# Optimization experiments

Hardware: AMD Instinct MI355X
Metric: run time of the kernel (lower is better)

The kernel has to match this reference:

```python
import jax, jax.numpy as jnp
import numpy as np

B, N, H, E_PER = 32, 128, 128, 4096  # graphs, nodes/graph, hidden_dim, pairs/graph


def setup_inputs() -> dict:
    key = jax.random.key(0)
    k1, k2, k3, k4, k5 = jax.random.split(key, 5)
    h_node = jax.random.normal(k1, (B, N, H), dtype=jnp.float32)
    h_edge = jax.random.normal(k2, (B, N, N, H), dtype=jnp.float32)
    # pairlist rows (b, i, j), grouped by batch index b as the torch loop assumes
    b = jnp.repeat(jnp.arange(B, dtype=jnp.int32), E_PER)
    i = jax.random.randint(k3, (B * E_PER,), 0, N, dtype=jnp.int32)
    j = jax.random.randint(k4, (B * E_PER,), 0, N, dtype=jnp.int32)
    pairlist = jnp.stack([b, i, j], axis=1)
    # foward_message_layer: Linear(3H, 6H); store weight transposed for x @ W
    W = jax.random.normal(k5, (3 * H, 6 * H), dtype=jnp.float32) / np.float32(np.sqrt(3 * H))
    bias = jnp.zeros((6 * H,), dtype=jnp.float32)
    return {"h_node": h_node, "h_edge": h_edge, "pairlist": pairlist, "W": W, "bias": bias}


def reference(h_node, h_edge, pairlist, W, bias):
    # Gather per-pair node/edge embeddings and concat: [E, 3H]
    bi, ii, jj = pairlist[:, 0], pairlist[:, 1], pairlist[:, 2]
    m = jnp.concatenate(
        [h_node[bi, ii], h_node[bi, jj], h_edge[bi, ii, jj]], axis=-1
    )
    # Shared linear message transform (Linear(3H, 6H)), then regroup per graph
    out = m @ W + bias  # [E, 6H]
    return out.reshape(B, E_PER, 6 * H)
```

## Files before the change

### kernel.cpp

```cpp
#include <hip/hip_runtime.h>


#define NNODE 128
#define HDIM  128
#define KDIM  384
#define NOUT  768
#define BM    128
#define BN    128
#define BK    64
#define NKITER 6

typedef __attribute__((ext_vector_type(4))) float f32x4;
typedef __attribute__((ext_vector_type(8))) short bf16x8;

static __device__ __forceinline__ short f2b(float f) {
    return __builtin_bit_cast(short, (__bf16)f);
}

static __device__ __forceinline__ void gload_lds16(const void* g, void* l) {
    __builtin_amdgcn_global_load_lds((const __attribute__((address_space(1))) void*)g,
                                     (__attribute__((address_space(3))) void*)l, 16, 0, 0);
}

__global__ void prep_kernel(const float* __restrict__ W, short* __restrict__ WtS) {
    int gid  = blockIdx.x * 256 + threadIdx.x;
    int tile = gid >> 10;
    int c    = gid & 1023;
    int nb   = tile / 6, kk = tile - nb * 6;
    int row  = c >> 3;
    int kb   = (c & 7) ^ (row & 7);
    int n    = nb * 128 + row;
    int k0   = kk * 64 + kb * 8;
    short v[8];
    #pragma unroll
    for (int e = 0; e < 8; ++e) v[e] = f2b(W[(k0 + e) * NOUT + n]);
    *(bf16x8*)(WtS + (size_t)gid * 8) = *(bf16x8*)v;
}

__global__ __launch_bounds__(256) void gemm_kernel(
    const float* __restrict__ h_node, const float* __restrict__ h_edge,
    const int* __restrict__ pl, const short* __restrict__ WtS,
    const float* __restrict__ bias, float* __restrict__ out) {

    __shared__ int rowOff[3][BM];
    __shared__ __align__(16) short Abuf[2][BM * BK];
    __shared__ __align__(16) short Bbuf[2][BN * BK];

    const int tid = threadIdx.x;
    const int bid = blockIdx.x;
    const int xcd = bid & 7;
    const int idx = bid >> 3;
    const int mBase = (xcd * 128 + idx / 6) * BM;
    const int nb    = idx % 6;
    const int nBase = nb * BN;
    const int nb6   = nb * 6;

    if (tid < BM) {
        int e  = pl ? mBase + tid : 0;
        int b  = pl[3 * (mBase + tid) + 0];
        int ii = pl[3 * (mBase + tid) + 1];
        int jj = pl[3 * (mBase + tid) + 2];
        (void)e;
        rowOff[0][tid] = (b * NNODE + ii) * HDIM;
        rowOff[1][tid] = (b * NNODE + jj) * HDIM;
        rowOff[2][tid] = ((b * NNODE + ii) * NNODE + jj) * HDIM;
    }
    __syncthreads();

    const int lane = tid & 63;
    const int wid  = tid >> 6;
    const int wm   = wid & 1;
    const int wn   = wid >> 1;
    const int r    = lane & 15;
    const int g    = lane >> 4;
    const int srow = tid >> 3;
    const int sc   = tid & 7;

    int ro[3][4];
    #pragma unroll
    for (int s = 0; s < 3; ++s)
        #pragma unroll
        for (int t = 0; t < 4; ++t)
            ro[s][t] = rowOff[s][srow + t * 32];

    f32x4 acc[4][4];
    #pragma unroll
    for (int a = 0; a < 4; ++a)
        #pragma unroll
        for (int b2 = 0; b2 < 4; ++b2)
            acc[a][b2] = (f32x4){0.f, 0.f, 0.f, 0.f};

    f32x4 a0[4], a1[4];

    auto issueA = [&](int kt) {
        const int seg  = kt >> 1;
        const float* gb = (seg < 2) ? h_node : h_edge;
        const int koff = (kt & 1) * BK;
        #pragma unroll
        for (int t = 0; t < 4; ++t) {
            const float* p = gb + ro[seg][t] + koff + sc * 8;
            a0[t] = *(const f32x4*)p;
            a1[t] = *(const f32x4*)(p + 4);
        }
    };
    auto issueB = [&](int kt, int buf) {
        const short* src = WtS + (size_t)((nb6 + kt) << 10) * 8;
        short* ldsb = &Bbuf[buf][0];
        #pragma unroll
        for (int i = 0; i < 4; ++i) {
            int cb0 = wid * 256 + i * 64;
            gload_lds16(src + (size_t)(cb0 + lane) * 8, ldsb + cb0 * 8);
        }
    };
    auto writeA = [&](int buf) {
        char* Ab = (char*)&Abuf[buf][0];
        #pragma unroll
        for (int t = 0; t < 4; ++t) {
            int row  = srow + t * 32;
            int byte = (row * 128 + sc * 16) ^ ((row & 7) << 4);
            bf16x8 v;
            v[0] = f2b(a0[t][0]); v[1] = f2b(a0[t][1]);
            v[2] = f2b(a0[t][2]); v[3] = f2b(a0[t][3]);
            v[4] = f2b(a1[t][0]); v[5] = f2b(a1[t][1]);
            v[6] = f2b(a1[t][2]); v[7] = f2b(a1[t][3]);
            *(bf16x8*)(Ab + byte) = v;
        }
    };
    auto compute = [&](int buf) {
        char* Ab = (char*)&Abuf[buf][0];
        char* Bb = (char*)&Bbuf[buf][0];
        #pragma unroll
        for (int ks = 0; ks < 2; ++ks) {
            const int cb = ks * 4 + g;
            bf16x8 ef[4], wf[4];
            #pragma unroll
            for (int mf = 0; mf < 4; ++mf) {
                int row  = wm * 64 + mf * 16 + r;
                int byte = (row * 128 + cb * 16) ^ ((row & 7) << 4);
                ef[mf] = *(const bf16x8*)(Ab + byte);
            }
            #pragma unroll
            for (int nf = 0; nf < 4; ++nf) {
                int row  = wn * 64 + nf * 16 + r;
                int byte = (row * 128 + cb * 16) ^ ((row & 7) << 4);
                wf[nf] = *(const bf16x8*)(Bb + byte);
            }
            #pragma unroll
            for (int nf = 0; nf < 4; ++nf)
                #pragma unroll
                for (int mf = 0; mf < 4; ++mf)
                    acc[nf][mf] = __builtin_amdgcn_mfma_f32_16x16x32_bf16(
                        wf[nf], ef[mf], acc[nf][mf], 0, 0, 0);
        }
    };

    issueA(0);
    issueB(0, 0);
    asm volatile("s_waitcnt vmcnt(0)" ::: "memory");
    writeA(0);
    __syncthreads();

    int cur = 0;
    #pragma unroll
    for (int t = 0; t < NKITER; ++t) {
        if (t + 1 < NKITER) {
            issueA(t + 1);
            issueB(t + 1, cur ^ 1);
        }
        compute(cur);
        if (t + 1 < NKITER) {
            asm volatile("s_waitcnt vmcnt(0)" ::: "memory");
            writeA(cur ^ 1);
            __syncthreads();
        }
        cur ^= 1;
    }

    #pragma unroll
    for (int nf = 0; nf < 4; ++nf) {
        int n = nBase + wn * 64 + nf * 16 + g * 4;
        f32x4 bb = *(const f32x4*)(bias + n);
        #pragma unroll
        for (int mf = 0; mf < 4; ++mf) {
            int m = mBase + wm * 64 + mf * 16 + r;
            f32x4 v = acc[nf][mf] + bb;
            *(f32x4*)(out + (size_t)m * NOUT + n) = v;
        }
    }
}

extern "C" void kernel_launch(void* const* d_in, const int* in_sizes, int n_in,
                              void* d_out, int out_size, void* d_ws, size_t ws_size,
                              hipStream_t stream) {
    const float* h_node = (const float*)d_in[0];
    const float* h_edge = (const float*)d_in[1];
    const int*   pl     = (const int*)d_in[2];
    const float* W      = (const float*)d_in[3];
    const float* bias   = (const float*)d_in[4];
    float* out = (float*)d_out;
    short* WtS = (short*)d_ws;

    prep_kernel<<<144, 256, 0, stream>>>(W, WtS);
    gemm_kernel<<<1024 * 6, 256, 0, stream>>>(h_node, h_edge, pl, WtS, bias, out);
}
```

Measured before the change: 636.1 us.

## Split gather into separate bf16 pre-pass and stage A via direct LDS loads

Result: slower. 662.4 us (+4.1%).

```diff
diff --git a/kernel.cpp b/kernel.cpp
--- a/kernel.cpp
+++ b/kernel.cpp
@@ -9,6 +9,7 @@
 #define BN    128
 #define BK    64
 #define NKITER 6
+#define MTOT  131072
 
 typedef __attribute__((ext_vector_type(4))) float f32x4;
 typedef __attribute__((ext_vector_type(8))) short bf16x8;
@@ -37,12 +38,33 @@
     *(bf16x8*)(WtS + (size_t)gid * 8) = *(bf16x8*)v;
 }
 
+__global__ __launch_bounds__(256) void gather_kernel(
+    const float* __restrict__ h_node, const float* __restrict__ h_edge,
+    const int* __restrict__ pl, short* __restrict__ Am) {
+    int cid = blockIdx.x * 256 + threadIdx.x;
+    int row = cid / 48;
+    int c   = cid - row * 48;
+    int b  = pl[3 * row + 0];
+    int ii = pl[3 * row + 1];
+    int jj = pl[3 * row + 2];
+    const float* base;
+    int seg = c >> 4;
+    if (seg == 0)      base = h_node + (b * NNODE + ii) * HDIM;
+    else if (seg == 1) base = h_node + (b * NNODE + jj) * HDIM;
+    else               base = h_edge + ((b * NNODE + ii) * NNODE + jj) * HDIM;
+    const float* p = base + (c & 15) * 8;
+    f32x4 x = *(const f32x4*)p;
+    f32x4 y = *(const f32x4*)(p + 4);
+    bf16x8 v;
+    v[0] = f2b(x[0]); v[1] = f2b(x[1]); v[2] = f2b(x[2]); v[3] = f2b(x[3]);
+    v[4] = f2b(y[0]); v[5] = f2b(y[1]); v[6] = f2b(y[2]); v[7] = f2b(y[3]);
+    *(bf16x8*)(Am + (size_t)row * KDIM + c * 8) = v;
+}
+
 __global__ __launch_bounds__(256) void gemm_kernel(
-    const float* __restrict__ h_node, const float* __restrict__ h_edge,
-    const int* __restrict__ pl, const short* __restrict__ WtS,
+    const short* __restrict__ Am, const short* __restrict__ WtS,
     const float* __restrict__ bias, float* __restrict__ out) {
 
-    __shared__ int rowOff[3][BM];
     __shared__ __align__(16) short Abuf[2][BM * BK];
     __shared__ __align__(16) short Bbuf[2][BN * BK];
 
@@ -55,33 +77,12 @@
     const int nBase = nb * BN;
     const int nb6   = nb * 6;
 
-    if (tid < BM) {
-        int e  = pl ? mBase + tid : 0;
-        int b  = pl[3 * (mBase + tid) + 0];
-        int ii = pl[3 * (mBase + tid) + 1];
-        int jj = pl[3 * (mBase + tid) + 2];
-        (void)e;
-        rowOff[0][tid] = (b * NNODE + ii) * HDIM;
-        rowOff[1][tid] = (b * NNODE + jj) * HDIM;
-        rowOff[2][tid] = ((b * NNODE + ii) * NNODE + jj) * HDIM;
-    }
-    __syncthreads();
-
     const int lane = tid & 63;
     const int wid  = tid >> 6;
     const int wm   = wid & 1;
     const int wn   = wid >> 1;
     const int r    = lane & 15;
     const int g    = lane >> 4;
-    const int srow = tid >> 3;
-    const int sc   = tid & 7;
-
-    int ro[3][4];
-    #pragma unroll
-    for (int s = 0; s < 3; ++s)
-        #pragma unroll
-        for (int t = 0; t < 4; ++t)
-            ro[s][t] = rowOff[s][srow + t * 32];
 
     f32x4 acc[4][4];
     #pragma unroll
@@ -90,40 +91,25 @@
         for (int b2 = 0; b2 < 4; ++b2)
             acc[a][b2] = (f32x4){0.f, 0.f, 0.f, 0.f};
 
-    f32x4 a0[4], a1[4];
-
-    auto issueA = [&](int kt) {
-        const int seg  = kt >> 1;
-        const float* gb = (seg < 2) ? h_node : h_edge;
-        const int koff = (kt & 1) * BK;
+    auto stageA = [&](int kt, int buf) {
+        short* ldsb = &Abuf[buf][0];
         #pragma unroll
-        for (int t = 0; t < 4; ++t) {
-            const float* p = gb + ro[seg][t] + koff + sc * 8;
-            a0[t] = *(const f32x4*)p;
-            a1[t] = *(const f32x4*)(p + 4);
+        for (int i = 0; i < 4; ++i) {
+            int cb0 = wid * 256 + i * 64;
+            int c   = cb0 + lane;
+            int row = c >> 3;
+            int kb  = (c & 7) ^ (row & 7);
+            const short* src = Am + (size_t)(mBase + row) * KDIM + kt * BK + kb * 8;
+            gload_lds16(src, ldsb + cb0 * 8);
         }
     };
-    auto issueB = [&](int kt, int buf) {
+    auto stageB = [&](int kt, int buf) {
         const short* src = WtS + (size_t)((nb6 + kt) << 10) * 8;
         short* ldsb = &Bbuf[buf][0];
         #pragma unroll
         for (int i = 0; i < 4; ++i) {
             int cb0 = wid * 256 + i * 64;
             gload_lds16(src + (size_t)(cb0 + lane) * 8, ldsb + cb0 * 8);
-        }
-    };
-    auto writeA = [&](int buf) {
-        char* Ab = (char*)&Abuf[buf][0];
-        #pragma unroll
-        for (int t = 0; t < 4; ++t) {
-            int row  = srow + t * 32;
-            int byte = (row * 128 + sc * 16) ^ ((row & 7) << 4);
-            bf16x8 v;
-            v[0] = f2b(a0[t][0]); v[1] = f2b(a0[t][1]);
-            v[2] = f2b(a0[t][2]); v[3] = f2b(a0[t][3]);
-            v[4] = f2b(a1[t][0]); v[5] = f2b(a1[t][1]);
-            v[6] = f2b(a1[t][2]); v[7] = f2b(a1[t][3]);
-            *(bf16x8*)(Ab + byte) = v;
         }
     };
     auto compute = [&](int buf) {
@@ -154,23 +140,23 @@
         }
     };
 
-    issueA(0);
-    issueB(0, 0);
+    stageA(0, 0);
+    stageB(0, 0);
     asm volatile("s_waitcnt vmcnt(0)" ::: "memory");
-    writeA(0);
     __syncthreads();
 
     int cur = 0;
     #pragma unroll
     for (int t = 0; t < NKITER; ++t) {
         if (t + 1 < NKITER) {
-            issueA(t + 1);
-            issueB(t + 1, cur ^ 1);
+            stageA(t + 1, cur ^ 1);
+            stageB(t + 1, cur ^ 1);
         }
+        __builtin_amdgcn_s_setprio(1);
         compute(cur);
+        __builtin_amdgcn_s_setprio(0);
         if (t + 1 < NKITER) {
             asm volatile("s_waitcnt vmcnt(0)" ::: "memory");
-            writeA(cur ^ 1);
             __syncthreads();
         }
         cur ^= 1;
@@ -199,7 +185,9 @@
     const float* bias   = (const float*)d_in[4];
     float* out = (float*)d_out;
     short* WtS = (short*)d_ws;
+    short* Am  = (short*)((char*)d_ws + (1 << 20));
 
     prep_kernel<<<144, 256, 0, stream>>>(W, WtS);
-    gemm_kernel<<<1024 * 6, 256, 0, stream>>>(h_node, h_edge, pl, WtS, bias, out);
+    gather_kernel<<<24576, 256, 0, stream>>>(h_node, h_edge, pl, Am);
+    gemm_kernel<<<1024 * 6, 256, 0, stream>>>(Am, WtS, bias, out);
 }
```
